# Performance work log

Hardware: AMD Instinct MI355X
Metric: run time of the kernel (lower is better)

The kernel has to match this reference:

```python
import jax, jax.numpy as jnp
import numpy as np

B, C, H, WID = 32, 64, 128, 128
K = 5            # co-occurrence bins (co_shape)
WH = 3           # spatial filter height/width (w_shape = (1,3,3), depth 1)
ACT_LO, ACT_HI = 0.0, 1.0  # actBounds


def setup_inputs() -> dict:
    key = jax.random.key(0)
    k1, k2, k3 = jax.random.split(key, 3)
    input_tensor = jax.random.uniform(k1, (B, C, H, WID), dtype=jnp.float32)
    # learned params: L ~ N(0, 0.1) of shape (k,k); W ~ N(0,0.1) of shape (d,h,w)
    L = 0.1 * jax.random.normal(k2, (K, K), dtype=jnp.float32)
    W = 0.1 * jax.random.normal(k3, (1, WH, WH), dtype=jnp.float32)
    return {"input_tensor": input_tensor, "W": W, "L": L}


def _quantize(x, k):
    # map activation in [ACT_LO, ACT_HI] to bin index in [0, k-1]
    b = jnp.floor((x - ACT_LO) / (ACT_HI - ACT_LO) * k)
    return jnp.clip(b, 0, k - 1).astype(jnp.int32)


def reference(input_tensor, W, L):
    """Co-occurrence layer:
    out[p] = sum_{q in 3x3 nbhd(p)} W[q-p] * L[bin(x[q]), bin(x[p])] * x[q]
    Out-of-bounds neighbors contribute 0 (zero pad => x[q]=0 kills the term),
    matching the precomputed neighbor_lookup_table boundary handling.
    """
    k = L.shape[0]
    pad = WH // 2
    bins = _quantize(input_tensor, k)                      # (B,C,H,W) int32
    xp = jnp.pad(input_tensor, ((0, 0), (0, 0), (pad, pad), (pad, pad)))
    bp = jnp.pad(bins, ((0, 0), (0, 0), (pad, pad), (pad, pad)))
    h, w = input_tensor.shape[2], input_tensor.shape[3]
    out = jnp.zeros_like(input_tensor)
    for dh in range(WH):                                   # tiny fixed 3x3 loop
        for dw in range(WH):
            xn = xp[:, :, dh:dh + h, dw:dw + w]            # shifted neighbor values
            bn = bp[:, :, dh:dh + h, dw:dw + w]            # shifted neighbor bins
            out = out + W[0, dh, dw] * L[bn, bins] * xn    # gather L + weighted acc
    return out
```

## Files before the change

kernel.cpp:

```cpp
#include <hip/hip_runtime.h>


namespace {
constexpr int H  = 128;
constexpr int WD = 128;
constexpr int PLANES = 32 * 64;
constexpr int PX  = 8;
constexpr int TPR = WD / PX;
constexpr int RPB = 32;
constexpr int THREADS = RPB * TPR;
constexpr int TILES = H / RPB;
}

__global__ __launch_bounds__(THREADS) void col_kernel(
    const float* __restrict__ x, const float* __restrict__ Wf,
    const float* __restrict__ Lf, float* __restrict__ out)
{
    __shared__ float WL[9 * 25];
    const int t = threadIdx.x;
    if (t < 225) WL[t] = Wf[t / 25] * Lf[t % 25];
    __syncthreads();

    const int plane = blockIdx.x >> 2;
    const int row   = ((blockIdx.x & 3) << 5) + (t >> 4);
    const int col0  = (t & 15) * PX;
    const float* xp = x + (size_t)plane * (H * WD);

    float win[3][PX + 2];
    #pragma unroll
    for (int dr = 0; dr < 3; ++dr) {
        const int rr = row + dr - 1;
        float4 c0 = make_float4(0.f, 0.f, 0.f, 0.f);
        float4 c1 = make_float4(0.f, 0.f, 0.f, 0.f);
        float l = 0.f, r = 0.f;
        if (rr >= 0 && rr < H) {
            const float* rp = xp + rr * WD + col0;
            c0 = *(const float4*)rp;
            c1 = *(const float4*)(rp + 4);
            if (col0 > 0)       l = rp[-1];
            if (col0 < WD - PX) r = rp[PX];
        }
        win[dr][0] = l;
        win[dr][1] = c0.x; win[dr][2] = c0.y; win[dr][3] = c0.z; win[dr][4] = c0.w;
        win[dr][5] = c1.x; win[dr][6] = c1.y; win[dr][7] = c1.z; win[dr][8] = c1.w;
        win[dr][9] = r;
    }

    const char* wlb = (const char*)WL;
    float acc[PX];
    #pragma unroll
    for (int i = 0; i < PX; ++i) acc[i] = 0.f;

    int bp4[PX];
    int b20[PX + 2];

    auto row_terms = [&](int drIdx, const float (&wr)[PX + 2]) {
        float tv[3][PX];
        #pragma unroll
        for (int dw = 0; dw < 3; ++dw)
            #pragma unroll
            for (int i = 0; i < PX; ++i)
                tv[dw][i] = *(const float*)(
                    wlb + (b20[i + dw] + bp4[i] + (drIdx * 3 + dw) * 100));
        #pragma unroll
        for (int dw = 0; dw < 3; ++dw)
            #pragma unroll
            for (int i = 0; i < PX; ++i)
                acc[i] = fmaf(tv[dw][i], wr[i + dw], acc[i]);
    };

    #pragma unroll
    for (int j = 0; j < PX + 2; ++j) {
        const int b  = (int)fminf(win[1][j] * 5.0f, 4.0f);
        const int b4 = b << 2;
        b20[j] = (b << 4) + b4;
        if (j >= 1 && j <= PX) bp4[j - 1] = b4;
    }
    row_terms(1, win[1]);

    #pragma unroll
    for (int j = 0; j < PX + 2; ++j) {
        const int b = (int)fminf(win[0][j] * 5.0f, 4.0f);
        b20[j] = (b << 4) + (b << 2);
    }
    row_terms(0, win[0]);

    #pragma unroll
    for (int j = 0; j < PX + 2; ++j) {
        const int b = (int)fminf(win[2][j] * 5.0f, 4.0f);
        b20[j] = (b << 4) + (b << 2);
    }
    row_terms(2, win[2]);

    float* op = out + (size_t)plane * (H * WD) + row * WD + col0;
    *(float4*)op       = make_float4(acc[0], acc[1], acc[2], acc[3]);
    *(float4*)(op + 4) = make_float4(acc[4], acc[5], acc[6], acc[7]);
}

extern "C" void kernel_launch(void* const* d_in, const int* in_sizes, int n_in,
                              void* d_out, int out_size, void* d_ws, size_t ws_size,
                              hipStream_t stream) {
    const float* x  = (const float*)d_in[0];
    const float* Wf = (const float*)d_in[1];
    const float* Lf = (const float*)d_in[2];
    float* out = (float*)d_out;

    col_kernel<<<dim3(PLANES * TILES), dim3(THREADS), 0, stream>>>(x, Wf, Lf, out);
}
```

Baseline: 257.5 us.

## Precompute combined three-neighbor lookup table to cut LDS gathers per pixel

Replaces the 9-entry W×L shared table with a 3×625 float4 table indexed by the three neighbor bins in a row plus the center bin. Each pixel then does three vectorized LDS loads instead of nine scalar ones. The cost is a much larger per-block table build: about 1875 entries with integer divisions and global reads. The table also uses roughly 30 KB of LDS per block, which may reduce occupancy and cause wider bank-conflicting accesses.

New measurement: 287.8 us. +11.8%, slower.

```diff
diff --git a/kernel.cpp b/kernel.cpp
--- a/kernel.cpp
+++ b/kernel.cpp
@@ -10,15 +10,31 @@
 constexpr int RPB = 32;
 constexpr int THREADS = RPB * TPR;
 constexpr int TILES = H / RPB;
+constexpr int TBL = 625;
 }
 
 __global__ __launch_bounds__(THREADS) void col_kernel(
     const float* __restrict__ x, const float* __restrict__ Wf,
     const float* __restrict__ Lf, float* __restrict__ out)
 {
-    __shared__ float WL[9 * 25];
+    __shared__ float4 T[3 * TBL];
+
     const int t = threadIdx.x;
-    if (t < 225) WL[t] = Wf[t / 25] * Lf[t % 25];
+
+    for (int e = t; e < 3 * TBL; e += THREADS) {
+        const int dr  = e / TBL;
+        const int rem = e - dr * TBL;
+        const int b0  = rem / 125;
+        const int b1  = (rem / 25) % 5;
+        const int b2  = (rem / 5) % 5;
+        const int bp  = rem % 5;
+        float4 v;
+        v.x = Wf[dr * 3 + 0] * Lf[b0 * 5 + bp];
+        v.y = Wf[dr * 3 + 1] * Lf[b1 * 5 + bp];
+        v.z = Wf[dr * 3 + 2] * Lf[b2 * 5 + bp];
+        v.w = 0.0f;
+        T[e] = v;
+    }
     __syncthreads();
 
     const int plane = blockIdx.x >> 2;
@@ -46,51 +62,42 @@
         win[dr][9] = r;
     }
 
-    const char* wlb = (const char*)WL;
     float acc[PX];
     #pragma unroll
     for (int i = 0; i < PX; ++i) acc[i] = 0.f;
 
-    int bp4[PX];
-    int b20[PX + 2];
+    const char* tb = (const char*)T;
+    int bp16[PX];
 
-    auto row_terms = [&](int drIdx, const float (&wr)[PX + 2]) {
-        float tv[3][PX];
+    auto do_row = [&](int drIdx) {
+        int A[PX + 2], Bc[PX + 2], Cc[PX + 2];
         #pragma unroll
-        for (int dw = 0; dw < 3; ++dw)
-            #pragma unroll
-            for (int i = 0; i < PX; ++i)
-                tv[dw][i] = *(const float*)(
-                    wlb + (b20[i + dw] + bp4[i] + (drIdx * 3 + dw) * 100));
+        for (int j = 0; j < PX + 2; ++j) {
+            const int b = (int)fminf(win[drIdx][j] * 5.0f, 4.0f);
+            A[j]  = b * 2000;
+            Bc[j] = b * 400;
+            Cc[j] = b * 80;
+            if (drIdx == 1) bp16[j > 0 ? j - 1 : 0] =
+                (j >= 1 && j <= PX) ? (b << 4) : bp16[0];
+        }
+        float4 tv[PX];
         #pragma unroll
-        for (int dw = 0; dw < 3; ++dw)
-            #pragma unroll
-            for (int i = 0; i < PX; ++i)
-                acc[i] = fmaf(tv[dw][i], wr[i + dw], acc[i]);
+        for (int i = 0; i < PX; ++i) {
+            const int addr = A[i] + Bc[i + 1] + Cc[i + 2] + bp16[i]
+                           + drIdx * (TBL * 16);
+            tv[i] = *(const float4*)(tb + addr);
+        }
+        #pragma unroll
+        for (int i = 0; i < PX; ++i) {
+            acc[i] = fmaf(tv[i].x, win[drIdx][i],     acc[i]);
+            acc[i] = fmaf(tv[i].y, win[drIdx][i + 1], acc[i]);
+            acc[i] = fmaf(tv[i].z, win[drIdx][i + 2], acc[i]);
+        }
     };
 
-    #pragma unroll
-    for (int j = 0; j < PX + 2; ++j) {
-        const int b  = (int)fminf(win[1][j] * 5.0f, 4.0f);
-        const int b4 = b << 2;
-        b20[j] = (b << 4) + b4;
-        if (j >= 1 && j <= PX) bp4[j - 1] = b4;
-    }
-    row_terms(1, win[1]);
-
-    #pragma unroll
-    for (int j = 0; j < PX + 2; ++j) {
-        const int b = (int)fminf(win[0][j] * 5.0f, 4.0f);
-        b20[j] = (b << 4) + (b << 2);
-    }
-    row_terms(0, win[0]);
-
-    #pragma unroll
-    for (int j = 0; j < PX + 2; ++j) {
-        const int b = (int)fminf(win[2][j] * 5.0f, 4.0f);
-        b20[j] = (b << 4) + (b << 2);
-    }
-    row_terms(2, win[2]);
+    do_row(1);
+    do_row(0);
+    do_row(2);
 
     float* op = out + (size_t)plane * (H * WD) + row * WD + col0;
     *(float4*)op       = make_float4(acc[0], acc[1], acc[2], acc[3]);
```
